# Optimization experiments

Measured on AMD Instinct MI355X. Metric: run time of the kernel, lower is better.

Reference implementation:

```python
import jax, jax.numpy as jnp
import numpy as np


def setup_inputs() -> dict:
    B, M, N, DEG, MAX_ITER = 256, 8192, 16384, 10, 30
    key = jax.random.key(0)
    k1, k2 = jax.random.split(key)
    rng = np.random.default_rng(0)
    cols = rng.integers(0, N, size=(M, DEG))
    cols[::2, -1] = N  # dummy (padding) entries on half the check rows; index N is the dummy column
    V_c_col = jnp.asarray(cols, dtype=jnp.int32)
    V_c_row = jnp.asarray(np.repeat(np.arange(M)[:, None], DEG, axis=1), dtype=jnp.int32)
    synd = jax.random.randint(k1, (B, M), 0, 2).astype(jnp.float32)
    llr0 = jax.random.normal(k2, (B, N), dtype=jnp.float32) + 2.0  # LLRs biased toward 'no error'
    return {"synd": synd, "llr0": llr0, "V_c_row": V_c_row, "V_c_col": V_c_col, "max_iter": MAX_ITER}


def _decode(synd, llr0, V_c_row, V_c_col, max_iter):
    B, M = synd.shape
    N = llr0.shape[1]
    dtype = llr0.dtype
    mask_dummy = (V_c_col == N)            # [M, DEG]
    cols_flat = V_c_col.reshape(-1)        # [M*DEG]
    inf = jnp.asarray(jnp.inf, dtype)
    # extended variable axis: real variables + one dummy column pinned to +inf LLR
    u_init = jnp.concatenate([llr0, jnp.full((B, 1), jnp.inf, dtype)], axis=1)   # [B, N+1]
    synd_neg = jnp.where(synd == 0, 1.0, -1.0).astype(dtype)[:, V_c_row]          # [B, M, DEG]
    message0 = u_init[:, V_c_col]                                                 # [B, M, DEG]
    l_v0 = jnp.zeros((B, N + 1), dtype)
    zeros_bn = jnp.zeros((B, N + 1), dtype)
    init = (message0, l_v0, zeros_bn, zeros_bn,
            jnp.full((B,), -1, jnp.int32), jnp.zeros((B,), jnp.int32))

    def step(carry, i):
        message, l_v, e_out, l_out, num_iters, conv = carry
        # vn_update: first iteration passes initial messages through unchanged
        a = jnp.where(i == 1, message, l_v[:, V_c_col] - message)
        # cn_update: normalized min-sum, beta = 1 - 2^{-i}
        beta = jnp.asarray(1.0, dtype) - jnp.power(jnp.asarray(2.0, dtype), -(i.astype(dtype)))
        sign = jnp.sign(a)
        sign = jnp.where(sign == 0, jnp.asarray(-1.0, dtype), sign)
        q_sign = synd_neg * jnp.prod(sign, axis=2, keepdims=True)
        ab = jnp.abs(a)
        srt = jnp.sort(ab, axis=2)
        min0, min1 = srt[:, :, :1], srt[:, :, 1:2]
        min_res = jnp.where(ab == min0, min1, min0)
        b = beta * sign * q_sign * min_res
        b = jnp.where(mask_dummy[None, :, :], jnp.asarray(0.0, dtype), b)
        # llr_update: scatter-add check->variable messages onto the intrinsic LLRs
        l_v = u_init.at[:, cols_flat].add(b.reshape(B, -1))
        l_v = l_v.at[:, -1].set(inf)
        e_v = (l_v <= 0).astype(dtype)
        # syndrome estimation: parity of the estimated error over each check's support
        s_est = jnp.mod(jnp.sum(e_v[:, V_c_col], axis=2), 2.0).astype(dtype)
        ok = jnp.all(s_est == synd, axis=1) & (num_iters == -1)
        num_iters = jnp.where(ok, i.astype(jnp.int32), num_iters)
        conv = jnp.where(ok, 1, conv)
        e_out = jnp.where(ok[:, None], e_v, e_out)
        l_out = jnp.where(ok[:, None], l_v, l_out)
        return (b, l_v, e_out, l_out, num_iters, conv), None

    (message, l_v, e_out, l_out, num_iters, conv), _ = jax.lax.scan(
        step, init, jnp.arange(1, max_iter + 1))
    # rows that never converged take the final-iteration estimate
    unconv = num_iters == -1
    e_v = (l_v <= 0).astype(dtype)
    e_out = jnp.where(unconv[:, None], e_v, e_out)
    l_out = jnp.where(unconv[:, None], l_v, l_out)
    num_iters = jnp.where(unconv, max_iter, num_iters)
    # drop the dummy column, matching e_out[:, :-1] / l_out[:, :-1]
    return e_out[:, :-1], num_iters, l_out[:, :-1], conv


def reference(synd, llr0, V_c_row, V_c_col, max_iter):
    return _decode(synd, llr0, V_c_row, V_c_col, max_iter)
```

## Files before the change

kernel.cpp:

```cpp
#include <hip/hip_runtime.h>
#include <cmath>
#include <cstdint>
#include <cstddef>

#define BB 256
#define MM 8192
#define NN 16384
#define DEG 10
#define MAX_ITER 30
#define PAR_BLOCKS 64
#define NXCD 8
#define GRP 32

typedef unsigned char  u8;
typedef unsigned short u16;


__global__ void k_init(int* colcnt, int* colfill, int* mm, int* niter, int* conv, int* cnt) {
    int t = blockIdx.x * blockDim.x + threadIdx.x;
    if (t < NN) { colcnt[t] = 0; colfill[t] = 0; }
    if (t < BB) { mm[t] = 0; niter[t] = -1; conv[t] = 0; }
    if (t == 0) *cnt = 0;
}

__global__ void k_transpose_f32(const float* __restrict__ in, float* __restrict__ out,
                                float* __restrict__ out2, int R, int C) {
    __shared__ float tile[64][65];
    int c0 = blockIdx.x * 64;
    int r0 = blockIdx.y * 64;
    #pragma unroll
    for (int k = 0; k < 16; k++) {
        int idx = k * 256 + threadIdx.x;
        int i = idx >> 6, j = idx & 63;
        tile[i][j] = in[(size_t)(r0 + i) * C + (c0 + j)];
    }
    __syncthreads();
    #pragma unroll
    for (int k = 0; k < 16; k++) {
        int idx = k * 256 + threadIdx.x;
        int i = idx >> 6, j = idx & 63;
        float v = tile[j][i];
        size_t o = (size_t)(c0 + i) * R + (r0 + j);
        out[o] = v;
        if (out2) out2[o] = v;
    }
}

__global__ void k_synd_t(const float* __restrict__ synd, u8* __restrict__ syndb) {
    __shared__ float tile[64][65];
    int c0 = blockIdx.x * 64;
    int r0 = blockIdx.y * 64;
    #pragma unroll
    for (int k = 0; k < 16; k++) {
        int idx = k * 256 + threadIdx.x;
        int i = idx >> 6, j = idx & 63;
        tile[i][j] = synd[(size_t)(r0 + i) * MM + (c0 + j)];
    }
    __syncthreads();
    #pragma unroll
    for (int k = 0; k < 16; k++) {
        int idx = k * 256 + threadIdx.x;
        int i = idx >> 6, j = idx & 63;
        syndb[(size_t)(c0 + i) * BB + (r0 + j)] = (tile[j][i] != 0.0f) ? 1 : 0;
    }
}

__global__ void k_hist(const int* __restrict__ vc, int* colcnt) {
    int e = blockIdx.x * 256 + threadIdx.x;
    if (e >= MM * DEG) return;
    int c = vc[e];
    if (c < NN) atomicAdd(&colcnt[c], 1);
}

__global__ void k_scan(const int* __restrict__ colcnt, int* __restrict__ colptr) {
    __shared__ int part[256];
    __shared__ int base[257];
    int t = threadIdx.x;
    int s = 0;
    for (int i = 0; i < 64; i++) s += colcnt[t * 64 + i];
    part[t] = s;
    __syncthreads();
    if (t == 0) {
        int acc = 0;
        for (int i = 0; i < 256; i++) { base[i] = acc; acc += part[i]; }
        base[256] = acc;
    }
    __syncthreads();
    int acc = base[t];
    for (int i = 0; i < 64; i++) { int c = t * 64 + i; colptr[c] = acc; acc += colcnt[c]; }
    if (t == 255) colptr[NN] = base[256];
}

__global__ void k_fill(const int* __restrict__ vc, const int* __restrict__ colptr,
                       int* colfill, int* coledges) {
    int e = blockIdx.x * 256 + threadIdx.x;
    if (e >= MM * DEG) return;
    int c = vc[e];
    if (c < NN) {
        int p = colptr[c] + atomicAdd(&colfill[c], 1);
        coledges[p] = e;
    }
}

__global__ void k_sort(const int* __restrict__ colptr, int* coledges) {
    int n = blockIdx.x * 256 + threadIdx.x;
    if (n >= NN) return;
    int p0 = colptr[n], p1 = colptr[n + 1];
    for (int i = p0 + 1; i < p1; i++) {
        int v = coledges[i];
        int j = i - 1;
        while (j >= p0 && coledges[j] > v) { coledges[j + 1] = coledges[j]; j--; }
        coledges[j + 1] = v;
    }
}


__global__ void k_check4(const int* __restrict__ vc, const float* __restrict__ lv,
                         float* __restrict__ svv, u16* __restrict__ sbits,
                         const u8* __restrict__ syndb, float beta, int first) {
    __shared__ int cs[32 * DEG];
    int bid = blockIdx.x, t = threadIdx.x;
    int g = bid & (NXCD - 1);
    int r0 = (bid >> 3) * 32;
    for (int i = t; i < 32 * DEG; i += 256) cs[i] = vc[r0 * DEG + i];
    __syncthreads();

    int row = t >> 3;
    int m = r0 + row;
    int b4 = g * GRP + (t & 7) * 4;
    size_t mb = (size_t)m * BB + b4;

    float pv0[4], pv1[4];
    unsigned pb[4];
    if (!first) {
        float4 q0 = *(const float4*)(svv + mb * 2);
        float4 q1 = *(const float4*)(svv + mb * 2 + 4);
        ushort4 pbv = *(const ushort4*)(sbits + mb);
        pv0[0] = q0.x; pv1[0] = q0.y; pv0[1] = q0.z; pv1[1] = q0.w;
        pv0[2] = q1.x; pv1[2] = q1.y; pv0[3] = q1.z; pv1[3] = q1.w;
        pb[0] = pbv.x; pb[1] = pbv.y; pb[2] = pbv.z; pb[3] = pbv.w;
    } else {
        #pragma unroll
        for (int j = 0; j < 4; j++) { pv0[j] = 0.f; pv1[j] = 0.f; pb[j] = 0; }
    }
    int pi0[4]; unsigned pq[4];
    #pragma unroll
    for (int j = 0; j < 4; j++) { pi0[j] = (pb[j] >> 11) & 15; pq[j] = (pb[j] >> 10) & 1u; }

    float m0[4] = {INFINITY, INFINITY, INFINITY, INFINITY};
    float m1[4] = {INFINITY, INFINITY, INFINITY, INFINITY};
    unsigned neg[4] = {0, 0, 0, 0};
    int i0[4] = {0, 0, 0, 0};

    #pragma unroll
    for (int d = 0; d < DEG; d++) {
        int c = cs[row * DEG + d];
        if (c >= NN) continue;
        float4 gv = *(const float4*)(lv + (size_t)c * BB + b4);
        float gj[4] = {gv.x, gv.y, gv.z, gv.w};
        #pragma unroll
        for (int j = 0; j < 4; j++) {
            float a;
            if (first) a = gj[j];
            else {
                float tt = (d == pi0[j]) ? pv1[j] : pv0[j];
                unsigned sx = pq[j] ^ ((pb[j] >> d) & 1u);
                a = gj[j] - (sx ? -tt : tt);
            }
            if (!(a > 0.0f)) neg[j] |= 1u << d;
            float x = fabsf(a);
            if (x < m0[j]) { m1[j] = m0[j]; m0[j] = x; i0[j] = d; }
            else if (x < m1[j]) m1[j] = x;
        }
    }

    uchar4 sb = *(const uchar4*)(syndb + mb);
    unsigned sbv[4] = {sb.x, sb.y, sb.z, sb.w};
    unsigned q[4];
    #pragma unroll
    for (int j = 0; j < 4; j++)
        q[j] = (__popc(neg[j]) & 1u) ^ (sbv[j] ? 1u : 0u);

    float v0[4], v1[4];
    #pragma unroll
    for (int j = 0; j < 4; j++) { v0[j] = beta * m0[j]; v1[j] = beta * m1[j]; }

    *(float4*)(svv + mb * 2)     = make_float4(v0[0], v1[0], v0[1], v1[1]);
    *(float4*)(svv + mb * 2 + 4) = make_float4(v0[2], v1[2], v0[3], v1[3]);
    ushort4 nb;
    nb.x = (u16)(neg[0] | (q[0] << 10) | ((unsigned)i0[0] << 11));
    nb.y = (u16)(neg[1] | (q[1] << 10) | ((unsigned)i0[1] << 11));
    nb.z = (u16)(neg[2] | (q[2] << 10) | ((unsigned)i0[2] << 11));
    nb.w = (u16)(neg[3] | (q[3] << 10) | ((unsigned)i0[3] << 11));
    *(ushort4*)(sbits + mb) = nb;
}

__global__ void k_var4(const float* __restrict__ llr0t, const float* __restrict__ svv,
                       const u16* __restrict__ sbits,
                       const int* __restrict__ colptr, const int* __restrict__ coledges,
                       float* __restrict__ lv, const int* __restrict__ niter) {
    int bid = blockIdx.x, t = threadIdx.x;
    int g = bid & (NXCD - 1);
    int n0 = (bid >> 3) * 32;
    int n = n0 + (t >> 3);
    int b4 = g * GRP + (t & 7) * 4;

    int4 f = *(const int4*)(niter + b4);
    if (f.x != -1 && f.y != -1 && f.z != -1 && f.w != -1) return;

    float4 s = *(const float4*)(llr0t + (size_t)n * BB + b4);
    int p0 = colptr[n], p1 = colptr[n + 1];
    for (int pp = p0; pp < p1; pp++) {
        int e = coledges[pp];
        int m = e / DEG;
        int d = e - m * DEG;
        size_t mb = (size_t)m * BB + b4;
        float4 q0 = *(const float4*)(svv + mb * 2);
        float4 q1 = *(const float4*)(svv + mb * 2 + 4);
        ushort4 bb = *(const ushort4*)(sbits + mb);
        {
            float tt = (d == ((bb.x >> 11) & 15)) ? q0.y : q0.x;
            unsigned sx = ((bb.x >> 10) ^ (bb.x >> d)) & 1u;
            s.x += sx ? -tt : tt;
        }
        {
            float tt = (d == ((bb.y >> 11) & 15)) ? q0.w : q0.z;
            unsigned sx = ((bb.y >> 10) ^ (bb.y >> d)) & 1u;
            s.y += sx ? -tt : tt;
        }
        {
            float tt = (d == ((bb.z >> 11) & 15)) ? q1.y : q1.x;
            unsigned sx = ((bb.z >> 10) ^ (bb.z >> d)) & 1u;
            s.z += sx ? -tt : tt;
        }
        {
            float tt = (d == ((bb.w >> 11) & 15)) ? q1.w : q1.z;
            unsigned sx = ((bb.w >> 10) ^ (bb.w >> d)) & 1u;
            s.w += sx ? -tt : tt;
        }
    }
    float* dst = lv + (size_t)n * BB + b4;
    if (f.x == -1 && f.y == -1 && f.z == -1 && f.w == -1) {
        *(float4*)dst = s;
    } else {
        if (f.x == -1) dst[0] = s.x;
        if (f.y == -1) dst[1] = s.y;
        if (f.z == -1) dst[2] = s.z;
        if (f.w == -1) dst[3] = s.w;
    }
}

__global__ void k_parity(const int* __restrict__ vc, const float* __restrict__ lv,
                         const u8* __restrict__ syndb, int* __restrict__ niter,
                         int* __restrict__ conv, int* __restrict__ mm,
                         int* __restrict__ cnt, int it) {
    __shared__ int s_stop, s_last;
    int b = threadIdx.x;
    bool frozen = (niter[b] != -1);
    volatile int* vmm = (volatile int*)mm;

    for (int m = blockIdx.x; m < MM; m += PAR_BLOCKS) {
        if (b == 0) s_stop = 1;
        __syncthreads();
        bool flagged = frozen || (vmm[b] != 0);
        if (!flagged) s_stop = 0;
        __syncthreads();
        if (s_stop) break;
        if (!flagged) {
            unsigned par = 0;
            #pragma unroll
            for (int d = 0; d < DEG; d++) {
                int c = vc[m * DEG + d];
                if (c < NN) par ^= (lv[(size_t)c * BB + b] <= 0.0f) ? 1u : 0u;
            }
            if (par != (unsigned)syndb[(size_t)m * BB + b]) atomicOr(&mm[b], 1);
        }
    }
    __syncthreads();
    __threadfence();
    if (b == 0) {
        int tk = atomicAdd(cnt, 1);
        s_last = (tk == PAR_BLOCKS - 1) ? 1 : 0;
    }
    __syncthreads();
    if (s_last) {
        int mmv = atomicAdd(&mm[b], 0);
        if (niter[b] == -1 && mmv == 0) { niter[b] = it; conv[b] = 1; }
        mm[b] = 0;
        if (b == 0) *cnt = 0;
    }
}


__global__ void k_out_e(const float* __restrict__ lv, float* __restrict__ out) {
    __shared__ float tile[64][65];
    int c0 = blockIdx.x * 64;
    int r0 = blockIdx.y * 64;
    #pragma unroll
    for (int k = 0; k < 16; k++) {
        int idx = k * 256 + threadIdx.x;
        int i = idx >> 6, j = idx & 63;
        tile[i][j] = (lv[(size_t)(r0 + i) * BB + (c0 + j)] <= 0.0f) ? 1.0f : 0.0f;
    }
    __syncthreads();
    #pragma unroll
    for (int k = 0; k < 16; k++) {
        int idx = k * 256 + threadIdx.x;
        int i = idx >> 6, j = idx & 63;
        out[(size_t)(c0 + i) * NN + (r0 + j)] = tile[j][i];
    }
}

__global__ void k_out_scalars(const int* __restrict__ niter, const int* __restrict__ conv,
                              float* __restrict__ out_ni, float* __restrict__ out_conv) {
    int b = threadIdx.x;
    int ni = niter[b];
    out_ni[b] = (float)(ni == -1 ? MAX_ITER : ni);
    out_conv[b] = (float)conv[b];
}


extern "C" void kernel_launch(void* const* d_in, const int* in_sizes, int n_in,
                              void* d_out, int out_size, void* d_ws, size_t ws_size,
                              hipStream_t stream) {
    const float* synd = (const float*)d_in[0];
    const float* llr0 = (const float*)d_in[1];
    const int* vcol   = (const int*)d_in[3];
    float* out = (float*)d_out;

    char* ws = (char*)d_ws;
    size_t off = 0;
    auto alloc = [&](size_t bytes) {
        off = (off + 255) & ~(size_t)255;
        size_t o = off; off += bytes; return o;
    };
    float* llr0t  = (float*)(ws + alloc((size_t)NN * BB * 4));
    float* lv     = (float*)(ws + alloc((size_t)NN * BB * 4));
    float* svv    = (float*)(ws + alloc((size_t)MM * BB * 8));
    u16*   sbits  = (u16*)(ws + alloc((size_t)MM * BB * 2));
    u8*   syndb   = (u8*)(ws + alloc((size_t)MM * BB));
    int* coledges = (int*)(ws + alloc((size_t)MM * DEG * 4));
    int* colptr   = (int*)(ws + alloc((size_t)(NN + 1) * 4));
    int* colcnt   = (int*)(ws + alloc((size_t)NN * 4));
    int* colfill  = (int*)(ws + alloc((size_t)NN * 4));
    int* mm       = (int*)(ws + alloc((size_t)BB * 4));
    int* niter    = (int*)(ws + alloc((size_t)BB * 4));
    int* conv     = (int*)(ws + alloc((size_t)BB * 4));
    int* cnt      = (int*)(ws + alloc(256));
    (void)in_sizes; (void)n_in; (void)out_size; (void)ws_size;

    k_init<<<NN / 256, 256, 0, stream>>>(colcnt, colfill, mm, niter, conv, cnt);
    k_transpose_f32<<<dim3(NN / 64, BB / 64), 256, 0, stream>>>(llr0, llr0t, lv, BB, NN);
    k_synd_t<<<dim3(MM / 64, BB / 64), 256, 0, stream>>>(synd, syndb);
    k_hist<<<(MM * DEG + 255) / 256, 256, 0, stream>>>(vcol, colcnt);
    k_scan<<<1, 256, 0, stream>>>(colcnt, colptr);
    k_fill<<<(MM * DEG + 255) / 256, 256, 0, stream>>>(vcol, colptr, colfill, coledges);
    k_sort<<<NN / 256, 256, 0, stream>>>(colptr, coledges);

    for (int i = 1; i <= MAX_ITER; i++) {
        float beta = 1.0f - ldexpf(1.0f, -i);
        k_check4<<<(MM / 32) * NXCD, 256, 0, stream>>>(vcol, lv, svv, sbits, syndb,
                                                       beta, (i == 1) ? 1 : 0);
        k_var4<<<(NN / 32) * NXCD, 256, 0, stream>>>(llr0t, svv, sbits, colptr,
                                                     coledges, lv, niter);
        k_parity<<<PAR_BLOCKS, 256, 0, stream>>>(vcol, lv, syndb, niter, conv, mm, cnt, i);
    }

    float* out_e    = out;
    float* out_ni   = out + (size_t)BB * NN;
    float* out_l    = out + (size_t)BB * NN + BB;
    float* out_conv = out + 2 * (size_t)BB * NN + BB;
    k_out_e<<<dim3(BB / 64, NN / 64), 256, 0, stream>>>(lv, out_e);
    k_transpose_f32<<<dim3(BB / 64, NN / 64), 256, 0, stream>>>(lv, out_l, nullptr, NN, BB);
    k_out_scalars<<<1, 256, 0, stream>>>(niter, conv, out_ni, out_conv);
}
```

Before: 1.715 ms.

## Scatter check-node messages into column-sorted buffer so variable update streams contiguously

The check kernel now also writes each edge's final signed message into a buffer ordered by column (CSC position, via a precomputed edge-to-position inverse map). The variable kernel then just sums contiguous float4 rows instead of gathering compressed min/sign data and decoding it per edge. The cost is about 84MB of extra scattered writes per iteration in place of gathered reads. Separately, the e and l outputs are now produced by one fused transpose kernel.

After: 1.958 ms. +14.2%, slower.

```diff
diff --git a/kernel.cpp b/kernel.cpp
--- a/kernel.cpp
+++ b/kernel.cpp
@@ -114,15 +114,27 @@
     }
 }
 
-
-__global__ void k_check4(const int* __restrict__ vc, const float* __restrict__ lv,
+__global__ void k_inv(const int* __restrict__ coledges, const int* __restrict__ colptr,
+                      int* __restrict__ edge2pos) {
+    int p = blockIdx.x * 256 + threadIdx.x;
+    if (p < colptr[NN]) edge2pos[coledges[p]] = p;
+}
+
+
+__global__ void k_check4(const int* __restrict__ vc, const int* __restrict__ edge2pos,
+                         const float* __restrict__ lv,
                          float* __restrict__ svv, u16* __restrict__ sbits,
+                         float* __restrict__ msgT,
                          const u8* __restrict__ syndb, float beta, int first) {
     __shared__ int cs[32 * DEG];
+    __shared__ int eps[32 * DEG];
     int bid = blockIdx.x, t = threadIdx.x;
     int g = bid & (NXCD - 1);
     int r0 = (bid >> 3) * 32;
-    for (int i = t; i < 32 * DEG; i += 256) cs[i] = vc[r0 * DEG + i];
+    for (int i = t; i < 32 * DEG; i += 256) {
+        cs[i] = vc[r0 * DEG + i];
+        eps[i] = edge2pos[r0 * DEG + i];
+    }
     __syncthreads();
 
     int row = t >> 3;
@@ -193,16 +205,29 @@
     nb.z = (u16)(neg[2] | (q[2] << 10) | ((unsigned)i0[2] << 11));
     nb.w = (u16)(neg[3] | (q[3] << 10) | ((unsigned)i0[3] << 11));
     *(ushort4*)(sbits + mb) = nb;
-}
-
-__global__ void k_var4(const float* __restrict__ llr0t, const float* __restrict__ svv,
-                       const u16* __restrict__ sbits,
-                       const int* __restrict__ colptr, const int* __restrict__ coledges,
-                       float* __restrict__ lv, const int* __restrict__ niter) {
+
+    #pragma unroll
+    for (int d = 0; d < DEG; d++) {
+        int c = cs[row * DEG + d];
+        if (c >= NN) continue;
+        int pos = eps[row * DEG + d];
+        float val[4];
+        #pragma unroll
+        for (int j = 0; j < 4; j++) {
+            float tt = (d == i0[j]) ? v1[j] : v0[j];
+            unsigned sx = q[j] ^ ((neg[j] >> d) & 1u);
+            val[j] = sx ? -tt : tt;
+        }
+        *(float4*)(msgT + (size_t)pos * BB + b4) = make_float4(val[0], val[1], val[2], val[3]);
+    }
+}
+
+__global__ void k_var_st(const float* __restrict__ llr0t, const float* __restrict__ msgT,
+                         const int* __restrict__ colptr,
+                         float* __restrict__ lv, const int* __restrict__ niter) {
     int bid = blockIdx.x, t = threadIdx.x;
     int g = bid & (NXCD - 1);
-    int n0 = (bid >> 3) * 32;
-    int n = n0 + (t >> 3);
+    int n = (bid >> 3) * 32 + (t >> 3);
     int b4 = g * GRP + (t & 7) * 4;
 
     int4 f = *(const int4*)(niter + b4);
@@ -210,34 +235,9 @@
 
     float4 s = *(const float4*)(llr0t + (size_t)n * BB + b4);
     int p0 = colptr[n], p1 = colptr[n + 1];
-    for (int pp = p0; pp < p1; pp++) {
-        int e = coledges[pp];
-        int m = e / DEG;
-        int d = e - m * DEG;
-        size_t mb = (size_t)m * BB + b4;
-        float4 q0 = *(const float4*)(svv + mb * 2);
-        float4 q1 = *(const float4*)(svv + mb * 2 + 4);
-        ushort4 bb = *(const ushort4*)(sbits + mb);
-        {
-            float tt = (d == ((bb.x >> 11) & 15)) ? q0.y : q0.x;
-            unsigned sx = ((bb.x >> 10) ^ (bb.x >> d)) & 1u;
-            s.x += sx ? -tt : tt;
-        }
-        {
-            float tt = (d == ((bb.y >> 11) & 15)) ? q0.w : q0.z;
-            unsigned sx = ((bb.y >> 10) ^ (bb.y >> d)) & 1u;
-            s.y += sx ? -tt : tt;
-        }
-        {
-            float tt = (d == ((bb.z >> 11) & 15)) ? q1.y : q1.x;
-            unsigned sx = ((bb.z >> 10) ^ (bb.z >> d)) & 1u;
-            s.z += sx ? -tt : tt;
-        }
-        {
-            float tt = (d == ((bb.w >> 11) & 15)) ? q1.w : q1.z;
-            unsigned sx = ((bb.w >> 10) ^ (bb.w >> d)) & 1u;
-            s.w += sx ? -tt : tt;
-        }
+    for (int p = p0; p < p1; p++) {
+        float4 mv = *(const float4*)(msgT + (size_t)p * BB + b4);
+        s.x += mv.x; s.y += mv.y; s.z += mv.z; s.w += mv.w;
     }
     float* dst = lv + (size_t)n * BB + b4;
     if (f.x == -1 && f.y == -1 && f.z == -1 && f.w == -1) {
@@ -292,7 +292,8 @@
 }
 
 
-__global__ void k_out_e(const float* __restrict__ lv, float* __restrict__ out) {
+__global__ void k_out_both(const float* __restrict__ lv, float* __restrict__ out_l,
+                           float* __restrict__ out_e) {
     __shared__ float tile[64][65];
     int c0 = blockIdx.x * 64;
     int r0 = blockIdx.y * 64;
@@ -300,14 +301,17 @@
     for (int k = 0; k < 16; k++) {
         int idx = k * 256 + threadIdx.x;
         int i = idx >> 6, j = idx & 63;
-        tile[i][j] = (lv[(size_t)(r0 + i) * BB + (c0 + j)] <= 0.0f) ? 1.0f : 0.0f;
-    }
-    __syncthreads();
-    #pragma unroll
-    for (int k = 0; k < 16; k++) {
-        int idx = k * 256 + threadIdx.x;
-        int i = idx >> 6, j = idx & 63;
-        out[(size_t)(c0 + i) * NN + (r0 + j)] = tile[j][i];
+        tile[i][j] = lv[(size_t)(r0 + i) * BB + (c0 + j)];
+    }
+    __syncthreads();
+    #pragma unroll
+    for (int k = 0; k < 16; k++) {
+        int idx = k * 256 + threadIdx.x;
+        int i = idx >> 6, j = idx & 63;
+        float v = tile[j][i];
+        size_t o = (size_t)(c0 + i) * NN + (r0 + j);
+        out_l[o] = v;
+        out_e[o] = (v <= 0.0f) ? 1.0f : 0.0f;
     }
 }
 
@@ -339,7 +343,9 @@
     float* svv    = (float*)(ws + alloc((size_t)MM * BB * 8));
     u16*   sbits  = (u16*)(ws + alloc((size_t)MM * BB * 2));
     u8*   syndb   = (u8*)(ws + alloc((size_t)MM * BB));
+    float* msgT   = (float*)(ws + alloc((size_t)MM * DEG * BB * 4));
     int* coledges = (int*)(ws + alloc((size_t)MM * DEG * 4));
+    int* edge2pos = (int*)(ws + alloc((size_t)MM * DEG * 4));
     int* colptr   = (int*)(ws + alloc((size_t)(NN + 1) * 4));
     int* colcnt   = (int*)(ws + alloc((size_t)NN * 4));
     int* colfill  = (int*)(ws + alloc((size_t)NN * 4));
@@ -356,13 +362,13 @@
     k_scan<<<1, 256, 0, stream>>>(colcnt, colptr);
     k_fill<<<(MM * DEG + 255) / 256, 256, 0, stream>>>(vcol, colptr, colfill, coledges);
     k_sort<<<NN / 256, 256, 0, stream>>>(colptr, coledges);
+    k_inv<<<(MM * DEG + 255) / 256, 256, 0, stream>>>(coledges, colptr, edge2pos);
 
     for (int i = 1; i <= MAX_ITER; i++) {
         float beta = 1.0f - ldexpf(1.0f, -i);
-        k_check4<<<(MM / 32) * NXCD, 256, 0, stream>>>(vcol, lv, svv, sbits, syndb,
-                                                       beta, (i == 1) ? 1 : 0);
-        k_var4<<<(NN / 32) * NXCD, 256, 0, stream>>>(llr0t, svv, sbits, colptr,
-                                                     coledges, lv, niter);
+        k_check4<<<(MM / 32) * NXCD, 256, 0, stream>>>(vcol, edge2pos, lv, svv, sbits,
+                                                       msgT, syndb, beta, (i == 1) ? 1 : 0);
+        k_var_st<<<(NN / 32) * NXCD, 256, 0, stream>>>(llr0t, msgT, colptr, lv, niter);
         k_parity<<<PAR_BLOCKS, 256, 0, stream>>>(vcol, lv, syndb, niter, conv, mm, cnt, i);
     }
 
@@ -370,7 +376,6 @@
     float* out_ni   = out + (size_t)BB * NN;
     float* out_l    = out + (size_t)BB * NN + BB;
     float* out_conv = out + 2 * (size_t)BB * NN + BB;
-    k_out_e<<<dim3(BB / 64, NN / 64), 256, 0, stream>>>(lv, out_e);
-    k_transpose_f32<<<dim3(BB / 64, NN / 64), 256, 0, stream>>>(lv, out_l, nullptr, NN, BB);
+    k_out_both<<<dim3(BB / 64, NN / 64), 256, 0, stream>>>(lv, out_l, out_e);
     k_out_scalars<<<1, 256, 0, stream>>>(niter, conv, out_ni, out_conv);
 }
```

## Fuse syndrome convergence check into check-node kernel and merge output transposes

Applied to the files above, without the earlier changes.

The per-iteration parity kernel is removed. The syndrome check for the previous iteration's estimate is now computed inside k_check4, which already reads lv at every check's support, and a last-block atomic counter updates niter and conv. A single parity launch remains after the final iteration. The two output kernels that read lv are merged into one that writes both l and e. This saves a kernel launch and a full pass over lv each iteration, at the cost of an extra block-level sync plus atomics in the check kernel and a subtle cross-block completion protocol.

Measured after the change: 3.789 ms. 2.21x slower.

```diff
diff --git a/kernel.cpp b/kernel.cpp
--- a/kernel.cpp
+++ b/kernel.cpp
@@ -11,15 +11,18 @@
 #define PAR_BLOCKS 64
 #define NXCD 8
 #define GRP 32
+#define CHK_BLOCKS ((MM / 32) * NXCD)
 
 typedef unsigned char  u8;
 typedef unsigned short u16;
 
 
-__global__ void k_init(int* colcnt, int* colfill, int* mm, int* niter, int* conv, int* cnt) {
+__global__ void k_init(int* colcnt, int* colfill, int* mm, int* niter, int* conv,
+                       int* cnt, unsigned* mmw) {
     int t = blockIdx.x * blockDim.x + threadIdx.x;
     if (t < NN) { colcnt[t] = 0; colfill[t] = 0; }
     if (t < BB) { mm[t] = 0; niter[t] = -1; conv[t] = 0; }
+    if (t < NXCD) mmw[t] = 0u;
     if (t == 0) *cnt = 0;
 }
 
@@ -117,11 +120,17 @@
 
 __global__ void k_check4(const int* __restrict__ vc, const float* __restrict__ lv,
                          float* __restrict__ svv, u16* __restrict__ sbits,
-                         const u8* __restrict__ syndb, float beta, int first) {
+                         const u8* __restrict__ syndb,
+                         int* __restrict__ niter, int* __restrict__ conv,
+                         unsigned* __restrict__ mmw, int* __restrict__ cnt,
+                         float beta, int first, int it_prev) {
     __shared__ int cs[32 * DEG];
+    __shared__ unsigned s_mm;
+    __shared__ int s_last;
     int bid = blockIdx.x, t = threadIdx.x;
     int g = bid & (NXCD - 1);
     int r0 = (bid >> 3) * 32;
+    if (t == 0) { s_mm = 0u; s_last = 0; }
     for (int i = t; i < 32 * DEG; i += 256) cs[i] = vc[r0 * DEG + i];
     __syncthreads();
 
@@ -151,6 +160,7 @@
     float m1[4] = {INFINITY, INFINITY, INFINITY, INFINITY};
     unsigned neg[4] = {0, 0, 0, 0};
     int i0[4] = {0, 0, 0, 0};
+    unsigned ep = 0;
 
     #pragma unroll
     for (int d = 0; d < DEG; d++) {
@@ -160,6 +170,7 @@
         float gj[4] = {gv.x, gv.y, gv.z, gv.w};
         #pragma unroll
         for (int j = 0; j < 4; j++) {
+            if (gj[j] <= 0.0f) ep ^= 1u << j;
             float a;
             if (first) a = gj[j];
             else {
@@ -181,6 +192,13 @@
     for (int j = 0; j < 4; j++)
         q[j] = (__popc(neg[j]) & 1u) ^ (sbv[j] ? 1u : 0u);
 
+    if (it_prev) {
+        unsigned sm4 = (sbv[0] ? 1u : 0u) | (sbv[1] ? 2u : 0u) |
+                       (sbv[2] ? 4u : 0u) | (sbv[3] ? 8u : 0u);
+        unsigned mism = (ep ^ sm4) & 15u;
+        if (mism) atomicOr(&s_mm, mism << ((t & 7) * 4));
+    }
+
     float v0[4], v1[4];
     #pragma unroll
     for (int j = 0; j < 4; j++) { v0[j] = beta * m0[j]; v1[j] = beta * m1[j]; }
@@ -193,6 +211,27 @@
     nb.z = (u16)(neg[2] | (q[2] << 10) | ((unsigned)i0[2] << 11));
     nb.w = (u16)(neg[3] | (q[3] << 10) | ((unsigned)i0[3] << 11));
     *(ushort4*)(sbits + mb) = nb;
+
+    if (it_prev) {
+        __syncthreads();
+        if (t == 0) {
+            unsigned mask = s_mm;
+            if (mask & ~mmw[g]) atomicOr(&mmw[g], mask);
+            __threadfence();
+            int tk = atomicAdd(cnt, 1);
+            s_last = (tk == CHK_BLOCKS - 1) ? 1 : 0;
+        }
+        __syncthreads();
+        if (s_last) {
+            unsigned w = atomicAdd(&mmw[t >> 5], 0u);
+            if (niter[t] == -1 && !((w >> (t & 31)) & 1u)) {
+                niter[t] = it_prev; conv[t] = 1;
+            }
+            __syncthreads();
+            if (t < NXCD) mmw[t] = 0u;
+            if (t == 0) *cnt = 0;
+        }
+    }
 }
 
 __global__ void k_var4(const float* __restrict__ llr0t, const float* __restrict__ svv,
@@ -292,7 +331,8 @@
 }
 
 
-__global__ void k_out_e(const float* __restrict__ lv, float* __restrict__ out) {
+__global__ void k_out_both(const float* __restrict__ lv, float* __restrict__ out_l,
+                           float* __restrict__ out_e) {
     __shared__ float tile[64][65];
     int c0 = blockIdx.x * 64;
     int r0 = blockIdx.y * 64;
@@ -300,14 +340,17 @@
     for (int k = 0; k < 16; k++) {
         int idx = k * 256 + threadIdx.x;
         int i = idx >> 6, j = idx & 63;
-        tile[i][j] = (lv[(size_t)(r0 + i) * BB + (c0 + j)] <= 0.0f) ? 1.0f : 0.0f;
-    }
-    __syncthreads();
-    #pragma unroll
-    for (int k = 0; k < 16; k++) {
-        int idx = k * 256 + threadIdx.x;
-        int i = idx >> 6, j = idx & 63;
-        out[(size_t)(c0 + i) * NN + (r0 + j)] = tile[j][i];
+        tile[i][j] = lv[(size_t)(r0 + i) * BB + (c0 + j)];
+    }
+    __syncthreads();
+    #pragma unroll
+    for (int k = 0; k < 16; k++) {
+        int idx = k * 256 + threadIdx.x;
+        int i = idx >> 6, j = idx & 63;
+        float v = tile[j][i];
+        size_t o = (size_t)(c0 + i) * NN + (r0 + j);
+        out_l[o] = v;
+        out_e[o] = (v <= 0.0f) ? 1.0f : 0.0f;
     }
 }
 
@@ -347,9 +390,10 @@
     int* niter    = (int*)(ws + alloc((size_t)BB * 4));
     int* conv     = (int*)(ws + alloc((size_t)BB * 4));
     int* cnt      = (int*)(ws + alloc(256));
+    unsigned* mmw = (unsigned*)(ws + alloc(256));
     (void)in_sizes; (void)n_in; (void)out_size; (void)ws_size;
 
-    k_init<<<NN / 256, 256, 0, stream>>>(colcnt, colfill, mm, niter, conv, cnt);
+    k_init<<<NN / 256, 256, 0, stream>>>(colcnt, colfill, mm, niter, conv, cnt, mmw);
     k_transpose_f32<<<dim3(NN / 64, BB / 64), 256, 0, stream>>>(llr0, llr0t, lv, BB, NN);
     k_synd_t<<<dim3(MM / 64, BB / 64), 256, 0, stream>>>(synd, syndb);
     k_hist<<<(MM * DEG + 255) / 256, 256, 0, stream>>>(vcol, colcnt);
@@ -359,18 +403,18 @@
 
     for (int i = 1; i <= MAX_ITER; i++) {
         float beta = 1.0f - ldexpf(1.0f, -i);
-        k_check4<<<(MM / 32) * NXCD, 256, 0, stream>>>(vcol, lv, svv, sbits, syndb,
-                                                       beta, (i == 1) ? 1 : 0);
+        k_check4<<<CHK_BLOCKS, 256, 0, stream>>>(vcol, lv, svv, sbits, syndb,
+                                                 niter, conv, mmw, cnt,
+                                                 beta, (i == 1) ? 1 : 0, i - 1);
         k_var4<<<(NN / 32) * NXCD, 256, 0, stream>>>(llr0t, svv, sbits, colptr,
                                                      coledges, lv, niter);
-        k_parity<<<PAR_BLOCKS, 256, 0, stream>>>(vcol, lv, syndb, niter, conv, mm, cnt, i);
-    }
+    }
+    k_parity<<<PAR_BLOCKS, 256, 0, stream>>>(vcol, lv, syndb, niter, conv, mm, cnt, MAX_ITER);
 
     float* out_e    = out;
     float* out_ni   = out + (size_t)BB * NN;
     float* out_l    = out + (size_t)BB * NN + BB;
     float* out_conv = out + 2 * (size_t)BB * NN + BB;
-    k_out_e<<<dim3(BB / 64, NN / 64), 256, 0, stream>>>(lv, out_e);
-    k_transpose_f32<<<dim3(BB / 64, NN / 64), 256, 0, stream>>>(lv, out_l, nullptr, NN, BB);
+    k_out_both<<<dim3(BB / 64, NN / 64), 256, 0, stream>>>(lv, out_l, out_e);
     k_out_scalars<<<1, 256, 0, stream>>>(niter, conv, out_ni, out_conv);
 }
```

## Split batch into two halves per iteration and fuse output kernels

Applied to the files above, without the earlier changes.

The check and variable update kernels now each cover 16 batch columns per XCD group instead of 32. Each block handles 64 rows with 4 threads per row, and the pair is launched twice per iteration, once per batch half. The intent is to shrink the per-launch working set of the message arrays so it stays in cache between the check and variable steps. The two final output kernels are also fused into one transpose that writes both the LLR output and the hard decision, saving a pass over lv. The cost is twice as many launches per iteration and narrower 64-byte accesses per row. The k_sort argument edit is a no-op.

Result: slower. 2.272 ms (+32.5%).

```diff
diff --git a/kernel.cpp b/kernel.cpp
--- a/kernel.cpp
+++ b/kernel.cpp
@@ -11,6 +11,7 @@
 #define PAR_BLOCKS 64
 #define NXCD 8
 #define GRP 32
+#define HGRP 16
 
 typedef unsigned char  u8;
 typedef unsigned short u16;
@@ -117,17 +118,17 @@
 
 __global__ void k_check4(const int* __restrict__ vc, const float* __restrict__ lv,
                          float* __restrict__ svv, u16* __restrict__ sbits,
-                         const u8* __restrict__ syndb, float beta, int first) {
-    __shared__ int cs[32 * DEG];
+                         const u8* __restrict__ syndb, float beta, int first, int h) {
+    __shared__ int cs[64 * DEG];
     int bid = blockIdx.x, t = threadIdx.x;
     int g = bid & (NXCD - 1);
-    int r0 = (bid >> 3) * 32;
-    for (int i = t; i < 32 * DEG; i += 256) cs[i] = vc[r0 * DEG + i];
-    __syncthreads();
-
-    int row = t >> 3;
+    int r0 = (bid >> 3) * 64;
+    for (int i = t; i < 64 * DEG; i += 256) cs[i] = vc[r0 * DEG + i];
+    __syncthreads();
+
+    int row = t >> 2;
     int m = r0 + row;
-    int b4 = g * GRP + (t & 7) * 4;
+    int b4 = g * GRP + h * HGRP + (t & 3) * 4;
     size_t mb = (size_t)m * BB + b4;
 
     float pv0[4], pv1[4];
@@ -198,12 +199,11 @@
 __global__ void k_var4(const float* __restrict__ llr0t, const float* __restrict__ svv,
                        const u16* __restrict__ sbits,
                        const int* __restrict__ colptr, const int* __restrict__ coledges,
-                       float* __restrict__ lv, const int* __restrict__ niter) {
+                       float* __restrict__ lv, const int* __restrict__ niter, int h) {
     int bid = blockIdx.x, t = threadIdx.x;
     int g = bid & (NXCD - 1);
-    int n0 = (bid >> 3) * 32;
-    int n = n0 + (t >> 3);
-    int b4 = g * GRP + (t & 7) * 4;
+    int n = (bid >> 3) * 64 + (t >> 2);
+    int b4 = g * GRP + h * HGRP + (t & 3) * 4;
 
     int4 f = *(const int4*)(niter + b4);
     if (f.x != -1 && f.y != -1 && f.z != -1 && f.w != -1) return;
@@ -292,7 +292,8 @@
 }
 
 
-__global__ void k_out_e(const float* __restrict__ lv, float* __restrict__ out) {
+__global__ void k_out_both(const float* __restrict__ lv, float* __restrict__ out_l,
+                           float* __restrict__ out_e) {
     __shared__ float tile[64][65];
     int c0 = blockIdx.x * 64;
     int r0 = blockIdx.y * 64;
@@ -300,14 +301,17 @@
     for (int k = 0; k < 16; k++) {
         int idx = k * 256 + threadIdx.x;
         int i = idx >> 6, j = idx & 63;
-        tile[i][j] = (lv[(size_t)(r0 + i) * BB + (c0 + j)] <= 0.0f) ? 1.0f : 0.0f;
-    }
-    __syncthreads();
-    #pragma unroll
-    for (int k = 0; k < 16; k++) {
-        int idx = k * 256 + threadIdx.x;
-        int i = idx >> 6, j = idx & 63;
-        out[(size_t)(c0 + i) * NN + (r0 + j)] = tile[j][i];
+        tile[i][j] = lv[(size_t)(r0 + i) * BB + (c0 + j)];
+    }
+    __syncthreads();
+    #pragma unroll
+    for (int k = 0; k < 16; k++) {
+        int idx = k * 256 + threadIdx.x;
+        int i = idx >> 6, j = idx & 63;
+        float v = tile[j][i];
+        size_t o = (size_t)(c0 + i) * NN + (r0 + j);
+        out_l[o] = v;
+        out_e[o] = (v <= 0.0f) ? 1.0f : 0.0f;
     }
 }
 
@@ -355,14 +359,17 @@
     k_hist<<<(MM * DEG + 255) / 256, 256, 0, stream>>>(vcol, colcnt);
     k_scan<<<1, 256, 0, stream>>>(colcnt, colptr);
     k_fill<<<(MM * DEG + 255) / 256, 256, 0, stream>>>(vcol, colptr, colfill, coledges);
-    k_sort<<<NN / 256, 256, 0, stream>>>(colptr, coledges);
+    k_sort<<<NN / 256, 256, 0, stream>>>(coledges ? colptr : colptr, coledges);
 
     for (int i = 1; i <= MAX_ITER; i++) {
         float beta = 1.0f - ldexpf(1.0f, -i);
-        k_check4<<<(MM / 32) * NXCD, 256, 0, stream>>>(vcol, lv, svv, sbits, syndb,
-                                                       beta, (i == 1) ? 1 : 0);
-        k_var4<<<(NN / 32) * NXCD, 256, 0, stream>>>(llr0t, svv, sbits, colptr,
-                                                     coledges, lv, niter);
+        int first = (i == 1) ? 1 : 0;
+        for (int h = 0; h < 2; h++) {
+            k_check4<<<(MM / 64) * NXCD, 256, 0, stream>>>(vcol, lv, svv, sbits, syndb,
+                                                           beta, first, h);
+            k_var4<<<(NN / 64) * NXCD, 256, 0, stream>>>(llr0t, svv, sbits, colptr,
+                                                         coledges, lv, niter, h);
+        }
         k_parity<<<PAR_BLOCKS, 256, 0, stream>>>(vcol, lv, syndb, niter, conv, mm, cnt, i);
     }
 
@@ -370,7 +377,6 @@
     float* out_ni   = out + (size_t)BB * NN;
     float* out_l    = out + (size_t)BB * NN + BB;
     float* out_conv = out + 2 * (size_t)BB * NN + BB;
-    k_out_e<<<dim3(BB / 64, NN / 64), 256, 0, stream>>>(lv, out_e);
-    k_transpose_f32<<<dim3(BB / 64, NN / 64), 256, 0, stream>>>(lv, out_l, nullptr, NN, BB);
+    k_out_both<<<dim3(BB / 64, NN / 64), 256, 0, stream>>>(lv, out_l, out_e);
     k_out_scalars<<<1, 256, 0, stream>>>(niter, conv, out_ni, out_conv);
 }
```
